# Optimization experiments

Hardware: AMD Instinct MI355X
Metric: run time of the kernel (lower is better)

## Reference

```python
import jax, jax.numpy as jnp
import numpy as np

B, T, N, C, H = 2, 8, 256, 1024, 16
HD = C // H
NEG = jnp.float32(-1e30)


def _rope_tables(n_pos, head_dim):
    half = head_dim // 2
    inv = 1.0 / (10000.0 ** (np.arange(half, dtype=np.float64) / half))
    ang = np.arange(n_pos, dtype=np.float64)[:, None] * inv[None, :]  # [S, half]
    # repeat so cos/sin pair up with interleaved (even, odd) rotate-half pairs
    cos = np.repeat(np.cos(ang), 2, axis=-1).astype(np.float32)
    sin = np.repeat(np.sin(ang), 2, axis=-1).astype(np.float32)
    return jnp.asarray(cos), jnp.asarray(sin)


def setup_inputs() -> dict:
    key = jax.random.key(0)
    k = jax.random.split(key, 6)
    img = jax.random.normal(k[0], (B, T, N, C), jnp.float32)
    cam = jax.random.normal(k[1], (B, T, C), jnp.float32)
    w_qkv = 0.02 * jax.random.normal(k[2], (C, 3 * C), jnp.float32)
    w_proj = 0.02 * jax.random.normal(k[3], (C, C), jnp.float32)
    b_proj = jnp.zeros((C,), jnp.float32)
    cos_img, sin_img = _rope_tables(T * N, HD)
    cos_cam, sin_cam = _rope_tables(T, HD)
    # frame-causal mask for cam queries over fused [cam_t, img_t] KV blocks
    kv_frame = jnp.arange(T * (N + 1)) // (N + 1)          # [T*(N+1)]
    attn_mask = (kv_frame[None, :] <= jnp.arange(T)[:, None])[None, None]  # [1,1,T,T*(N+1)] bool
    return {"img": img, "cam": cam, "w_qkv": w_qkv, "w_proj": w_proj,
            "b_proj": b_proj, "cos_img": cos_img, "sin_img": sin_img,
            "cos_cam": cos_cam, "sin_cam": sin_cam, "attn_mask": attn_mask}


def _rotate_half(x):
    xp = x.reshape(x.shape[:-1] + (-1, 2))
    return jnp.stack((-xp[..., 1], xp[..., 0]), axis=-1).reshape(x.shape)


def _apply_rope(x, cos, sin):
    # x: [B,H,S,D]; cos/sin: [S,D]
    return x * cos[None, None] + _rotate_half(x) * sin[None, None]


def _qkv(x, w_qkv, num_heads):
    b, s, c = x.shape
    hd = c // num_heads
    qkv = (x @ w_qkv).reshape(b, s, 3, num_heads, hd)
    qkv = qkv.transpose(0, 3, 2, 1, 4)  # [B,H,3,S,hd]
    return qkv[:, :, 0], qkv[:, :, 1], qkv[:, :, 2]


def _sdpa(q, k, v, mask=None):
    scale = q.shape[-1] ** -0.5
    s = jnp.einsum('bhqd,bhkd->bhqk', q, k) * scale
    if mask is not None:
        s = jnp.where(mask, s, NEG)
    a = jax.nn.softmax(s, axis=-1)
    return jnp.einsum('bhqk,bhkd->bhqd', a, v)


def reference(img, cam, w_qkv, w_proj, b_proj, cos_img, sin_img, cos_cam, sin_cam, attn_mask):
    b, t, n, c = img.shape
    hd = cos_img.shape[-1]
    h = c // hd

    q_img, k_img, v_img = _qkv(img.reshape(b, t * n, c), w_qkv, h)
    q_img = _apply_rope(q_img, cos_img, sin_img)
    k_img = _apply_rope(k_img, cos_img, sin_img)

    q_cam, k_cam, v_cam = _qkv(cam, w_qkv, h)
    q_cam = _apply_rope(q_cam, cos_cam, sin_cam)
    k_cam = _apply_rope(k_cam, cos_cam, sin_cam)

    k_img = k_img.reshape(b, h, t, n, hd)
    v_img = v_img.reshape(b, h, t, n, hd)
    k_fused = jnp.concatenate([k_cam[:, :, :, None], k_img], axis=-2).reshape(b, h, t * (n + 1), hd)
    v_fused = jnp.concatenate([v_cam[:, :, :, None], v_img], axis=-2).reshape(b, h, t * (n + 1), hd)

    x_img = _sdpa(q_img, k_fused, v_fused).transpose(0, 2, 1, 3).reshape(b, t, n, c)
    x_cam = _sdpa(q_cam, k_fused, v_fused, mask=attn_mask).transpose(0, 2, 1, 3).reshape(b, t, c)

    img_out = x_img @ w_proj + b_proj
    cam_out = x_cam @ w_proj + b_proj
    return img_out, cam_out
```

## Files before the change

### kernel.cpp

```cpp
#include <hip/hip_runtime.h>

#define T_ 8
#define N_ 256
#define C_ 1024
#define H_ 16
#define D_ 64
#define U_ 2056
#define UPAD_ 2112
#define MROWS_ 4112
#define MPAD_ 4224
#define IMG_OUT_ELEMS 4194304

typedef __attribute__((ext_vector_type(4))) float f32x4;
typedef __attribute__((ext_vector_type(8))) short s16x8;
typedef __attribute__((ext_vector_type(4))) short s16x4;

__device__ __forceinline__ short f2bf(float f) {
  union { float f; unsigned u; } a; a.f = f;
  unsigned u = a.u;
  return (short)((u + 0x7fffu + ((u >> 16) & 1u)) >> 16);
}

__device__ __forceinline__ float b2f(short s) {
  union { unsigned u; float f; } a;
  a.u = ((unsigned)(unsigned short)s) << 16;
  return a.f;
}

__device__ __forceinline__ float exp2a(float x) {
  float r; asm("v_exp_f32 %0, %1" : "=v"(r) : "v"(x)); return r;
}

__device__ __forceinline__ unsigned cvt_pk_bf16(float lo, float hi) {
  unsigned r; asm("v_cvt_pk_bf16_f32 %0, %1, %2" : "=v"(r) : "v"(lo), "v"(hi)); return r;
}

#define ASYNC_COPY16(gp, lp)                                                   \
  __builtin_amdgcn_global_load_lds((const __attribute__((address_space(1))) void*)(gp), \
                                   (__attribute__((address_space(3))) void*)(lp), 16, 0, 0)

constexpr size_t OFF_XB     = 0;
constexpr size_t OFF_WQKVT  = OFF_XB + 8650752;
constexpr size_t OFF_WPROJT = OFF_WQKVT + 6291456;
constexpr size_t OFF_Q      = OFF_WPROJT + 2097152;
constexpr size_t OFF_K      = OFF_Q + 8421376;
constexpr size_t OFF_V      = OFF_K + 8650752;
constexpr size_t OFF_VT     = OFF_V + 8650752;
constexpr size_t OFF_X      = OFF_VT + 8650752;

__global__ __launch_bounds__(256) void prep_kernel(const float* __restrict__ img,
                                                   const float* __restrict__ cam,
                                                   short* __restrict__ Xb,
                                                   const float* __restrict__ wqkv,
                                                   short* __restrict__ Wqkvt,
                                                   const float* __restrict__ wproj,
                                                   short* __restrict__ Wprojt) {
  __shared__ float tile[32][33];
  const int bid = blockIdx.x;
  if (bid < 4112) {
    int gt = bid * 256 + threadIdx.x;
    int e = gt << 2;
    int row = e >> 10, col = e & 1023;
    int b = row / U_, u = row % U_, t = u / 257, jj = u % 257;
    const float* src = jj ? (img + ((size_t)((b * 8 + t) * 256 + (jj - 1)) << 10))
                          : (cam + ((size_t)(b * 8 + t) << 10));
    float4 f = *(const float4*)(src + col);
    s16x4 o;
    o[0] = f2bf(f.x); o[1] = f2bf(f.y); o[2] = f2bf(f.z); o[3] = f2bf(f.w);
    *(s16x4*)(Xb + ((size_t)row << 10) + col) = o;
    return;
  }
  const float* in; short* out; int Cc, bx, by;
  if (bid < 4112 + 3072) {
    int i = bid - 4112; bx = i % 96; by = i / 96; in = wqkv; out = Wqkvt; Cc = 3072;
  } else {
    int i = bid - 7184; bx = i % 32; by = i / 32; in = wproj; out = Wprojt; Cc = 1024;
  }
  constexpr int R = 1024;
  int tx = threadIdx.x & 31, ty = threadIdx.x >> 5;
  int col0 = bx << 5, row0 = by << 5;
#pragma unroll
  for (int i = 0; i < 4; i++) {
    int r = ty + i * 8;
    tile[r][tx] = in[(size_t)(row0 + r) * Cc + col0 + tx];
  }
  __syncthreads();
#pragma unroll
  for (int i = 0; i < 4; i++) {
    int r = ty + i * 8;
    out[(size_t)(col0 + r) * R + row0 + tx] = f2bf(tile[tx][r]);
  }
}

template <int EPI>
__global__ __launch_bounds__(256) void gemm_kernel(
    const short* __restrict__ A, const short* __restrict__ Bt,
    const float* __restrict__ cosi, const float* __restrict__ sini,
    const float* __restrict__ cosc, const float* __restrict__ sinc,
    short* __restrict__ qb, short* __restrict__ kb, short* __restrict__ vb,
    const float* __restrict__ bias, float* __restrict__ outp) {
  constexpr int K = 1024;
  __shared__ __align__(16) short As[128 * 32];
  __shared__ __align__(16) short Bs[128 * 32];
  const int tid = threadIdx.x, w = tid >> 6, lane = tid & 63;
  const int l16 = lane & 15, quad = lane >> 4;
  const int bn = blockIdx.x, bm = blockIdx.y;
  const f32x4 zero = {0.f, 0.f, 0.f, 0.f};
  f32x4 acc[4][4];
#pragma unroll
  for (int i = 0; i < 4; i++)
#pragma unroll
    for (int j = 0; j < 4; j++) acc[i][j] = zero;

  const int mb = (w >> 1) << 6, nb = (w & 1) << 6;

  for (int kb0 = 0; kb0 < K; kb0 += 32) {
    __syncthreads();
#pragma unroll
    for (int i = 0; i < 2; i++) {
      int row = (w << 5) + (i << 4) + (lane >> 2);
      int cseg = (lane & 3) << 3;
      const short* ga = A + (size_t)(bm * 128 + row) * K + kb0 + cseg;
      char* la = (char*)As + ((w << 5) + (i << 4)) * 64 + lane * 16;
      ASYNC_COPY16(ga, la);
      const short* gb = Bt + (size_t)(bn * 128 + row) * K + kb0 + cseg;
      char* lb = (char*)Bs + ((w << 5) + (i << 4)) * 64 + lane * 16;
      ASYNC_COPY16(gb, lb);
    }
    __syncthreads();
    s16x8 af[4], bf[4];
#pragma unroll
    for (int mi = 0; mi < 4; mi++)
      af[mi] = *(const s16x8*)&As[(mb + mi * 16 + l16) * 32 + quad * 8];
#pragma unroll
    for (int ni = 0; ni < 4; ni++)
      bf[ni] = *(const s16x8*)&Bs[(nb + ni * 16 + l16) * 32 + quad * 8];
#pragma unroll
    for (int mi = 0; mi < 4; mi++)
#pragma unroll
      for (int ni = 0; ni < 4; ni++)
        acc[mi][ni] = __builtin_amdgcn_mfma_f32_16x16x32_bf16(af[mi], bf[ni], acc[mi][ni], 0, 0, 0);
  }

#pragma unroll
  for (int mi = 0; mi < 4; mi++) {
#pragma unroll
    for (int ni = 0; ni < 4; ni++) {
#pragma unroll
      for (int reg = 0; reg < 4; reg++) {
        float val = acc[mi][ni][reg];
        float partner = __shfl_xor(val, 1, 64);
        int R = bm * 128 + mb + mi * 16 + quad * 4 + reg;
        int Cg = bn * 128 + nb + ni * 16 + l16;
        int b = R / U_;
        if (b < 2) {
          int u = R % U_, t = u / 257, jj = u % 257;
          if constexpr (EPI == 0) {
            int which = Cg >> 10, hc = Cg & 1023, h = hc >> 6, d = hc & 63;
            int bh = b * 16 + h;
            if (which == 2) {
              vb[((size_t)bh * UPAD_ + u) * 64 + d] = f2bf(val);
            } else {
              const float *ct, *st; int pos;
              if (jj == 0) { ct = cosc; st = sinc; pos = t; }
              else         { ct = cosi; st = sini; pos = u - t - 1; }
              float cv = ct[pos * 64 + d], sv = st[pos * 64 + d];
              float o = val * cv + ((d & 1) ? partner : -partner) * sv;
              if (which == 0) {
                o *= 0.18033688f;
                qb[((size_t)bh * U_ + u) * 64 + d] = f2bf(o);
              } else {
                kb[((size_t)bh * UPAD_ + u) * 64 + d] = f2bf(o);
              }
            }
          } else {
            float o = val + bias[Cg];
            if (jj) outp[(size_t)((b * 8 + t) * 256 + jj - 1) * 1024 + Cg] = o;
            else    outp[IMG_OUT_ELEMS + (size_t)(b * 8 + t) * 1024 + Cg] = o;
          }
        }
      }
    }
  }
}

__global__ __launch_bounds__(256) void attn_kernel(const short* __restrict__ q,
                                                   const short* __restrict__ k,
                                                   const short* __restrict__ vt,
                                                   short* __restrict__ x) {
  __shared__ __align__(16) short Kt[64 * 64];
  __shared__ __align__(16) short Vt[64 * 64];
  __shared__ __align__(16) short Pt[4 * 16 * 72];
  const int tid = threadIdx.x, w = tid >> 6, lane = tid & 63;
  const int l16 = lane & 15, quad = lane >> 4;
  const int flat = blockIdx.x;
  const int slot = flat >> 3;
  const int bh = ((flat & 7) << 2) + (slot >> 5);
  const int qt = slot & 31;
  const int b = bh >> 4, h = bh & 15;

  const int g = qt * 64 + w * 16 + l16;
  const int u_q = g + (g >> 8) + 1;
  const short* qp = q + ((size_t)bh * U_ + u_q) * 64;
  const s16x8 aq0 = *(const s16x8*)(qp + quad * 8);
  const s16x8 aq1 = *(const s16x8*)(qp + 32 + quad * 8);

  const int sr = w * 8 + (lane >> 3);
  const int c8 = lane & 7;
  const short* kg = k + ((size_t)bh * UPAD_ + sr) * 64 + (c8 << 3);
  const short* vg = vt + ((size_t)bh * 64 + sr) * UPAD_ + (c8 << 3);
  const int swz = ((c8 ^ (sr & 7)) << 3);
  short* const wk0 = &Kt[sr * 64 + swz];
  short* const wk1 = &Kt[(sr + 32) * 64 + swz];
  short* const wv0 = &Vt[sr * 64 + swz];
  short* const wv1 = &Vt[(sr + 32) * 64 + swz];

  const int cK0 = (quad * 8) ^ ((l16 & 7) << 3);
  const int cK1 = (32 + quad * 8) ^ ((l16 & 7) << 3);
  short* const pw = Pt + (w * 16 + l16) * 72;

  const f32x4 zero = {0.f, 0.f, 0.f, 0.f};
  float m_r = -3e38f, l_r = 0.f;
  f32x4 o_acc[4];
#pragma unroll
  for (int r = 0; r < 4; r++) o_acc[r] = zero;

  s16x8 rk0 = *(const s16x8*)(kg);
  s16x8 rk1 = *(const s16x8*)(kg + 2048);
  s16x8 rv0 = *(const s16x8*)(vg);
  s16x8 rv1 = *(const s16x8*)(vg + 32 * UPAD_);
  kg += 64 * 64;
  vg += 64;

  for (int kv0 = 0; kv0 < U_; kv0 += 64) {
    __syncthreads();
    *(s16x8*)wk0 = rk0;
    *(s16x8*)wk1 = rk1;
    *(s16x8*)wv0 = rv0;
    *(s16x8*)wv1 = rv1;
    __syncthreads();
    if (kv0 + 64 < U_) {
      rk0 = *(const s16x8*)(kg);
      rk1 = *(const s16x8*)(kg + 2048);
      rv0 = *(const s16x8*)(vg);
      rv1 = *(const s16x8*)(vg + 32 * UPAD_);
      kg += 64 * 64;
      vg += 64;
    }

    f32x4 sT[4];
    __builtin_amdgcn_s_setprio(1);
#pragma unroll
    for (int ni = 0; ni < 4; ni++) {
      const s16x8 b0 = *(const s16x8*)&Kt[(ni * 16 + l16) * 64 + cK0];
      const s16x8 b1 = *(const s16x8*)&Kt[(ni * 16 + l16) * 64 + cK1];
      f32x4 z = __builtin_amdgcn_mfma_f32_16x16x32_bf16(b0, aq0, zero, 0, 0, 0);
      sT[ni] = __builtin_amdgcn_mfma_f32_16x16x32_bf16(b1, aq1, z, 0, 0, 0);
    }
    __builtin_amdgcn_s_setprio(0);

    if (kv0 == 2048) {
#pragma unroll
      for (int ni = 0; ni < 4; ni++) {
        if (ni > 0 || quad >= 2) {
          sT[ni][0] = -1e30f; sT[ni][1] = -1e30f;
          sT[ni][2] = -1e30f; sT[ni][3] = -1e30f;
        }
      }
    }

    float mx01 = fmaxf(fmaxf(sT[0][0], sT[0][1]), fmaxf(sT[0][2], sT[0][3]));
    float mx23 = fmaxf(fmaxf(sT[1][0], sT[1][1]), fmaxf(sT[1][2], sT[1][3]));
    float mx45 = fmaxf(fmaxf(sT[2][0], sT[2][1]), fmaxf(sT[2][2], sT[2][3]));
    float mx67 = fmaxf(fmaxf(sT[3][0], sT[3][1]), fmaxf(sT[3][2], sT[3][3]));
    float mx = fmaxf(fmaxf(mx01, mx23), fmaxf(mx45, mx67));
    mx = fmaxf(mx, __shfl_xor(mx, 16, 64));
    mx = fmaxf(mx, __shfl_xor(mx, 32, 64));

    if (__any(mx > m_r + 8.f)) {
      const float mnew = fmaxf(m_r, mx);
      const float al = exp2a(m_r - mnew);
      m_r = mnew;
      l_r *= al;
      float aR[4];
#pragma unroll
      for (int reg = 0; reg < 4; reg++) aR[reg] = __shfl(al, quad * 4 + reg, 64);
#pragma unroll
      for (int ni = 0; ni < 4; ni++)
#pragma unroll
        for (int reg = 0; reg < 4; reg++) o_acc[ni][reg] *= aR[reg];
    }

    float rs = 0.f;
#pragma unroll
    for (int ni = 0; ni < 4; ni++)
#pragma unroll
      for (int reg = 0; reg < 4; reg++) {
        const float p = exp2a(sT[ni][reg] - m_r);
        sT[ni][reg] = p;
        rs += p;
      }
    l_r += rs;

#pragma unroll
    for (int ni = 0; ni < 4; ni++) {
      uint2 pk;
      pk.x = cvt_pk_bf16(sT[ni][0], sT[ni][1]);
      pk.y = cvt_pk_bf16(sT[ni][2], sT[ni][3]);
      *(uint2*)&pw[ni * 16 + quad * 4] = pk;
    }

    __builtin_amdgcn_s_setprio(1);
#pragma unroll
    for (int ks = 0; ks < 2; ks++) {
      const s16x8 ap = *(const s16x8*)&pw[ks * 32 + quad * 8];
#pragma unroll
      for (int ni = 0; ni < 4; ni++) {
        const s16x8 bv = *(const s16x8*)&Vt[(ni * 16 + l16) * 64 + (ks ? cK1 : cK0)];
        o_acc[ni] = __builtin_amdgcn_mfma_f32_16x16x32_bf16(ap, bv, o_acc[ni], 0, 0, 0);
      }
    }
    __builtin_amdgcn_s_setprio(0);
  }

  l_r += __shfl_xor(l_r, 16, 64);
  l_r += __shfl_xor(l_r, 32, 64);
  const float linv = 1.f / l_r;
  float lR[4];
#pragma unroll
  for (int reg = 0; reg < 4; reg++) lR[reg] = __shfl(linv, quad * 4 + reg, 64);

#pragma unroll
  for (int reg = 0; reg < 4; reg++) {
    const int go = qt * 64 + w * 16 + quad * 4 + reg;
    const int u_o = go + (go >> 8) + 1;
#pragma unroll
    for (int ni = 0; ni < 4; ni++)
      x[((size_t)(b * U_ + u_o)) * 1024 + h * 64 + ni * 16 + l16] =
          f2bf(o_acc[ni][reg] * lR[reg]);
  }
}

__global__ __launch_bounds__(256) void vtcam_kernel(const short* __restrict__ v,
                                                    short* __restrict__ vt,
                                                    const short* __restrict__ q,
                                                    const short* __restrict__ k,
                                                    short* __restrict__ x) {
  __shared__ __align__(16) char smem[16448];
  const int bid = blockIdx.x;
  const int tid = threadIdx.x;
  if (bid < 1056) {
    short (*t2)[65] = (short(*)[65])smem;
    int kt = bid % 33, bh = bid / 33;
#pragma unroll
    for (int i = 0; i < 16; i++) {
      int e = tid + i * 256; int r = e >> 6, c = e & 63;
      short vv = v[((size_t)bh * UPAD_ + kt * 64 + r) * 64 + c];
      t2[r][c] = (kt * 64 + r < U_) ? vv : (short)0;
    }
    __syncthreads();
#pragma unroll
    for (int i = 0; i < 16; i++) {
      int e = tid + i * 256; int d = e >> 6, c = e & 63;
      vt[((size_t)bh * 64 + d) * UPAD_ + kt * 64 + c] = t2[c][d];
    }
    return;
  }
  float* sb = (float*)smem;
  float* red = sb + U_;
  float (*obuf)[64] = (float(*)[64])(red + 8);
  const int i0 = bid - 1056;
  const int t = i0 & 7, bh = i0 >> 3;
  const int b = bh >> 4, h = bh & 15;
  const int L = (t + 1) * 257;
  const int lane = tid & 63, w = tid >> 6;
  const int u_q = t * 257;

  float qf[64];
  {
    const short* qpp = q + ((size_t)bh * U_ + u_q) * 64;
#pragma unroll
    for (int i = 0; i < 8; i++) {
      const s16x8 qv = *(const s16x8*)(qpp + i * 8);
#pragma unroll
      for (int j = 0; j < 8; j++) qf[i * 8 + j] = b2f(qv[j]);
    }
  }

  float lm = -3e38f;
  for (int kv = tid; kv < L; kv += 256) {
    const short* kp = k + ((size_t)bh * UPAD_ + kv) * 64;
    float s = 0.f;
#pragma unroll
    for (int i = 0; i < 8; i++) {
      const s16x8 kvv = *(const s16x8*)(kp + i * 8);
#pragma unroll
      for (int j = 0; j < 8; j++) s += qf[i * 8 + j] * b2f(kvv[j]);
    }
    sb[kv] = s;
    lm = fmaxf(lm, s);
  }
#pragma unroll
  for (int d = 1; d < 64; d <<= 1) lm = fmaxf(lm, __shfl_xor(lm, d, 64));
  if (lane == 0) red[w] = lm;
  __syncthreads();
  const float m = fmaxf(fmaxf(red[0], red[1]), fmaxf(red[2], red[3]));

  float ls = 0.f;
  for (int kv = tid; kv < L; kv += 256) {
    const float p = exp2a(sb[kv] - m);
    sb[kv] = p;
    ls += p;
  }
#pragma unroll
  for (int d = 1; d < 64; d <<= 1) ls += __shfl_xor(ls, d, 64);
  if (lane == 0) red[4 + w] = ls;
  __syncthreads();
  const float linv = 1.f / (red[4] + red[5] + red[6] + red[7]);

  const int d0 = (tid & 7) << 3;
  const int slot = tid >> 3;
  float acc[8];
#pragma unroll
  for (int j = 0; j < 8; j++) acc[j] = 0.f;
  for (int kv = slot; kv < L; kv += 32) {
    const float p = sb[kv];
    const s16x8 vv = *(const s16x8*)(v + ((size_t)bh * UPAD_ + kv) * 64 + d0);
#pragma unroll
    for (int j = 0; j < 8; j++) acc[j] += p * b2f(vv[j]);
  }
#pragma unroll
  for (int j = 0; j < 8; j++) obuf[slot][d0 + j] = acc[j];
  __syncthreads();
  if (tid < 64) {
    float s = 0.f;
#pragma unroll
    for (int i = 0; i < 32; i++) s += obuf[i][tid];
    x[((size_t)(b * U_ + u_q)) * 1024 + h * 64 + tid] = f2bf(s * linv);
  }
}

extern "C" void kernel_launch(void* const* d_in, const int* in_sizes, int n_in,
                              void* d_out, int out_size, void* d_ws, size_t ws_size,
                              hipStream_t stream) {
  const float* img   = (const float*)d_in[0];
  const float* cam   = (const float*)d_in[1];
  const float* wqkv  = (const float*)d_in[2];
  const float* wproj = (const float*)d_in[3];
  const float* bias  = (const float*)d_in[4];
  const float* cosi  = (const float*)d_in[5];
  const float* sini  = (const float*)d_in[6];
  const float* cosc  = (const float*)d_in[7];
  const float* sinc  = (const float*)d_in[8];
  float* outp = (float*)d_out;

  char* ws = (char*)d_ws;
  short* Xb     = (short*)(ws + OFF_XB);
  short* Wqkvt  = (short*)(ws + OFF_WQKVT);
  short* Wprojt = (short*)(ws + OFF_WPROJT);
  short* qb     = (short*)(ws + OFF_Q);
  short* kb     = (short*)(ws + OFF_K);
  short* vb     = (short*)(ws + OFF_V);
  short* vtb    = (short*)(ws + OFF_VT);
  short* xb     = (short*)(ws + OFF_X);

  prep_kernel<<<8208, 256, 0, stream>>>(img, cam, Xb, wqkv, Wqkvt, wproj, Wprojt);
  gemm_kernel<0><<<dim3(24, 33), 256, 0, stream>>>(Xb, Wqkvt, cosi, sini, cosc, sinc,
                                                   qb, kb, vb, nullptr, nullptr);
  vtcam_kernel<<<1312, 256, 0, stream>>>(vb, vtb, qb, kb, xb);
  attn_kernel<<<1024, 256, 0, stream>>>(qb, kb, vtb, xb);
  gemm_kernel<1><<<dim3(8, 33), 256, 0, stream>>>(xb, Wprojt, nullptr, nullptr, nullptr, nullptr,
                                                  nullptr, nullptr, nullptr, bias, outp);
}
```

Before: 312.5 us.

## Double-buffer GEMM LDS tiles, remap blocks per XCD, streamline epilogue indexing

```diff
diff --git a/kernel.cpp b/kernel.cpp
--- a/kernel.cpp
+++ b/kernel.cpp
@@ -100,11 +100,19 @@
     short* __restrict__ qb, short* __restrict__ kb, short* __restrict__ vb,
     const float* __restrict__ bias, float* __restrict__ outp) {
   constexpr int K = 1024;
-  __shared__ __align__(16) short As[128 * 32];
-  __shared__ __align__(16) short Bs[128 * 32];
+  __shared__ __align__(16) short As[2][128 * 32];
+  __shared__ __align__(16) short Bs[2][128 * 32];
   const int tid = threadIdx.x, w = tid >> 6, lane = tid & 63;
   const int l16 = lane & 15, quad = lane >> 4;
-  const int bn = blockIdx.x, bm = blockIdx.y;
+
+  int bn, bm;
+  {
+    const int flat = blockIdx.x;
+    const int xcd = flat & 7, idx = flat >> 3;
+    if constexpr (EPI == 0) { bn = xcd * 3 + idx / 33; bm = idx % 33; }
+    else                    { bn = xcd;                bm = idx;       }
+  }
+
   const f32x4 zero = {0.f, 0.f, 0.f, 0.f};
   f32x4 acc[4][4];
 #pragma unroll
@@ -114,57 +122,71 @@
 
   const int mb = (w >> 1) << 6, nb = (w & 1) << 6;
 
+  const int srow = (w << 5) + (lane >> 2);
+  const int cseg = (lane & 3) << 3;
+  const short* gA = A + (size_t)(bm * 128 + srow) * K + cseg;
+  const short* gB = Bt + (size_t)(bn * 128 + srow) * K + cseg;
+  const int lo0 = ((w << 5) << 6) + lane * 16;
+  const int lo1 = lo0 + (16 << 6);
+
+#define STAGE(buf, kb0)                                                        \
+  do {                                                                         \
+    ASYNC_COPY16(gA + (kb0), (char*)As[buf] + lo0);                            \
+    ASYNC_COPY16(gA + (size_t)16 * K + (kb0), (char*)As[buf] + lo1);           \
+    ASYNC_COPY16(gB + (kb0), (char*)Bs[buf] + lo0);                            \
+    ASYNC_COPY16(gB + (size_t)16 * K + (kb0), (char*)Bs[buf] + lo1);           \
+  } while (0)
+
+  STAGE(0, 0);
+  int cur = 0;
   for (int kb0 = 0; kb0 < K; kb0 += 32) {
     __syncthreads();
-#pragma unroll
-    for (int i = 0; i < 2; i++) {
-      int row = (w << 5) + (i << 4) + (lane >> 2);
-      int cseg = (lane & 3) << 3;
-      const short* ga = A + (size_t)(bm * 128 + row) * K + kb0 + cseg;
-      char* la = (char*)As + ((w << 5) + (i << 4)) * 64 + lane * 16;
-      ASYNC_COPY16(ga, la);
-      const short* gb = Bt + (size_t)(bn * 128 + row) * K + kb0 + cseg;
-      char* lb = (char*)Bs + ((w << 5) + (i << 4)) * 64 + lane * 16;
-      ASYNC_COPY16(gb, lb);
-    }
-    __syncthreads();
+    if (kb0 + 32 < K) STAGE(cur ^ 1, kb0 + 32);
     s16x8 af[4], bf[4];
 #pragma unroll
     for (int mi = 0; mi < 4; mi++)
-      af[mi] = *(const s16x8*)&As[(mb + mi * 16 + l16) * 32 + quad * 8];
+      af[mi] = *(const s16x8*)&As[cur][(mb + mi * 16 + l16) * 32 + quad * 8];
 #pragma unroll
     for (int ni = 0; ni < 4; ni++)
-      bf[ni] = *(const s16x8*)&Bs[(nb + ni * 16 + l16) * 32 + quad * 8];
+      bf[ni] = *(const s16x8*)&Bs[cur][(nb + ni * 16 + l16) * 32 + quad * 8];
 #pragma unroll
     for (int mi = 0; mi < 4; mi++)
 #pragma unroll
       for (int ni = 0; ni < 4; ni++)
         acc[mi][ni] = __builtin_amdgcn_mfma_f32_16x16x32_bf16(af[mi], bf[ni], acc[mi][ni], 0, 0, 0);
-  }
-
-#pragma unroll
-  for (int mi = 0; mi < 4; mi++) {
-#pragma unroll
-    for (int ni = 0; ni < 4; ni++) {
+    cur ^= 1;
+  }
+#undef STAGE
+
+  if constexpr (EPI == 0) {
+    const int cbase = bn * 128 + nb;
+    const int which = cbase >> 10;
+    const int hh = (cbase & 1023) >> 6;
+#pragma unroll
+    for (int mi = 0; mi < 4; mi++) {
 #pragma unroll
       for (int reg = 0; reg < 4; reg++) {
-        float val = acc[mi][ni][reg];
-        float partner = __shfl_xor(val, 1, 64);
-        int R = bm * 128 + mb + mi * 16 + quad * 4 + reg;
-        int Cg = bn * 128 + nb + ni * 16 + l16;
-        int b = R / U_;
-        if (b < 2) {
-          int u = R % U_, t = u / 257, jj = u % 257;
-          if constexpr (EPI == 0) {
-            int which = Cg >> 10, hc = Cg & 1023, h = hc >> 6, d = hc & 63;
-            int bh = b * 16 + h;
-            if (which == 2) {
-              vb[((size_t)bh * UPAD_ + u) * 64 + d] = f2bf(val);
-            } else {
-              const float *ct, *st; int pos;
-              if (jj == 0) { ct = cosc; st = sinc; pos = t; }
-              else         { ct = cosi; st = sini; pos = u - t - 1; }
-              float cv = ct[pos * 64 + d], sv = st[pos * 64 + d];
+        const int R = bm * 128 + mb + mi * 16 + quad * 4 + reg;
+        if (R < MROWS_) {
+          const int b = (R >= U_) ? 1 : 0;
+          const int u = R - b * U_;
+          const int t = (u - (u >> 8)) >> 8;
+          const int jj = u - ((t << 8) + t);
+          const int bh = b * 16 + hh;
+          if (which == 2) {
+#pragma unroll
+            for (int ni = 0; ni < 4; ni++)
+              vb[((size_t)bh * UPAD_ + u) * 64 + ni * 16 + l16] = f2bf(acc[mi][ni][reg]);
+          } else {
+            const float *ct, *st; int pos;
+            if (jj == 0) { ct = cosc; st = sinc; pos = t; }
+            else         { ct = cosi; st = sini; pos = u - t - 1; }
+#pragma unroll
+            for (int ni = 0; ni < 4; ni++) {
+              const int d = ni * 16 + l16;
+              const float val = acc[mi][ni][reg];
+              const float partner = __shfl_xor(val, 1, 64);
+              const float cv = ct[pos * 64 + d], sv = st[pos * 64 + d];
               float o = val * cv + ((d & 1) ? partner : -partner) * sv;
               if (which == 0) {
                 o *= 0.18033688f;
@@ -173,10 +195,29 @@
                 kb[((size_t)bh * UPAD_ + u) * 64 + d] = f2bf(o);
               }
             }
-          } else {
-            float o = val + bias[Cg];
-            if (jj) outp[(size_t)((b * 8 + t) * 256 + jj - 1) * 1024 + Cg] = o;
-            else    outp[IMG_OUT_ELEMS + (size_t)(b * 8 + t) * 1024 + Cg] = o;
+          }
+        }
+      }
+    }
+  } else {
+    const int cbase = bn * 128 + nb;
+#pragma unroll
+    for (int mi = 0; mi < 4; mi++) {
+#pragma unroll
+      for (int reg = 0; reg < 4; reg++) {
+        const int R = bm * 128 + mb + mi * 16 + quad * 4 + reg;
+        if (R < MROWS_) {
+          const int b = (R >= U_) ? 1 : 0;
+          const int u = R - b * U_;
+          const int t = (u - (u >> 8)) >> 8;
+          const int jj = u - ((t << 8) + t);
+          size_t rowoff;
+          if (jj) rowoff = (size_t)((b * 8 + t) * 256 + jj - 1) * 1024;
+          else    rowoff = IMG_OUT_ELEMS + (size_t)(b * 8 + t) * 1024;
+#pragma unroll
+          for (int ni = 0; ni < 4; ni++) {
+            const int Cg = cbase + ni * 16 + l16;
+            outp[rowoff + Cg] = acc[mi][ni][reg] + bias[Cg];
           }
         }
       }
@@ -465,10 +506,10 @@
   short* xb     = (short*)(ws + OFF_X);
 
   prep_kernel<<<8208, 256, 0, stream>>>(img, cam, Xb, wqkv, Wqkvt, wproj, Wprojt);
-  gemm_kernel<0><<<dim3(24, 33), 256, 0, stream>>>(Xb, Wqkvt, cosi, sini, cosc, sinc,
-                                                   qb, kb, vb, nullptr, nullptr);
+  gemm_kernel<0><<<792, 256, 0, stream>>>(Xb, Wqkvt, cosi, sini, cosc, sinc,
+                                          qb, kb, vb, nullptr, nullptr);
   vtcam_kernel<<<1312, 256, 0, stream>>>(vb, vtb, qb, kb, xb);
   attn_kernel<<<1024, 256, 0, stream>>>(qb, kb, vtb, xb);
-  gemm_kernel<1><<<dim3(8, 33), 256, 0, stream>>>(xb, Wprojt, nullptr, nullptr, nullptr, nullptr,
-                                                  nullptr, nullptr, nullptr, bias, outp);
-}
+  gemm_kernel<1><<<264, 256, 0, stream>>>(xb, Wprojt, nullptr, nullptr, nullptr, nullptr,
+                                          nullptr, nullptr, nullptr, bias, outp);
+}
```

Result: faster. 289.0 us (-7.5%).
